# Optimization experiments

Hardware: AMD Instinct MI355X
Metric: run time of the kernel (lower is better)

Reference implementation:

```python
import jax, jax.numpy as jnp
from jax import lax
import numpy as np

B, C, H, W = 8, 256, 128, 128
MID, RMID = C // 2, C // 4          # heatmap-head mid, radius-head mid channels
K = 5                                # K_max centers
THR = 0.1                            # nms_threshold
SMIN, SMAX = 0.05, 0.45              # sigma clamp
BETA = 1.5                           # prior aspect ratio sigma_y/sigma_x
DMAX = 0.08                          # sigma residual max
RMIN, RMAX = 0.03, 0.40              # radius range
BNEPS = 1e-5
PI = float(np.pi)


def setup_inputs() -> dict:
    key = jax.random.key(0)
    ks = jax.random.split(key, 12)
    def n(k, shp, s):
        return jax.random.normal(k, shp, dtype=jnp.float32) * s
    return {
        'x': n(ks[0], (B, C, H, W), 1.0),
        # heatmap head: DWConv3x3 -> PW1x1 -> BN/ReLU -> Conv3x3 -> BN/ReLU -> Conv1x1(+bias=-2) -> Sigmoid
        'hm_dw': n(ks[1], (C, 1, 3, 3), 0.1),
        'hm_pw1': n(ks[2], (MID, C, 1, 1), 0.05),
        'hm_g1': jnp.ones((MID,), jnp.float32), 'hm_b1': jnp.zeros((MID,), jnp.float32),
        'hm_c3': n(ks[3], (MID, MID, 3, 3), 0.05),
        'hm_g2': jnp.ones((MID,), jnp.float32), 'hm_b2': jnp.zeros((MID,), jnp.float32),
        'hm_out_w': n(ks[4], (1, MID, 1, 1), 0.2), 'hm_out_b': jnp.full((1,), -2.0, jnp.float32),
        # radius head: DWConv3x3 -> PW1x1 -> BN/ReLU -> Conv1x1(+bias) -> Sigmoid -> [r_min, r_max]
        'r_dw': n(ks[5], (C, 1, 3, 3), 0.1),
        'r_pw1': n(ks[6], (RMID, C, 1, 1), 0.05),
        'r_g': jnp.ones((RMID,), jnp.float32), 'r_b': jnp.zeros((RMID,), jnp.float32),
        'r_out_w': n(ks[7], (1, RMID, 1, 1), 0.1), 'r_out_b': jnp.zeros((1,), jnp.float32),
        # per-center param predictor
        'log_alpha': jnp.zeros((1,), jnp.float32),
        'mlp_w1': n(ks[8], (C, C // 2), 0.05), 'mlp_b1': jnp.zeros((C // 2,), jnp.float32),
        'mlp_w2': n(ks[9], (C // 2, 4), 0.05), 'mlp_b2': jnp.zeros((4,), jnp.float32),
    }


def conv(x, w, groups=1, pad=0):
    return lax.conv_general_dilated(x, w, (1, 1), [(pad, pad), (pad, pad)],
                                    dimension_numbers=('NCHW', 'OIHW', 'NCHW'),
                                    feature_group_count=groups)


def bn(x, g, b):
    # eval-mode BatchNorm with running_mean=0, running_var=1
    s = g / np.sqrt(1.0 + BNEPS)
    return x * s[:, None, None] + b[:, None, None]


def bilinear_sample(fm, cx, cy):
    # fm: (C,H,W); cx,cy: (K,) normalized in [-1,1]; align_corners=True, border padding
    px = jnp.clip((cx + 1.0) * 0.5 * (W - 1), 0.0, W - 1)
    py = jnp.clip((cy + 1.0) * 0.5 * (H - 1), 0.0, H - 1)
    x0 = jnp.floor(px).astype(jnp.int32); x1 = jnp.minimum(x0 + 1, W - 1)
    y0 = jnp.floor(py).astype(jnp.int32); y1 = jnp.minimum(y0 + 1, H - 1)
    wx = px - x0; wy = py - y0
    v00 = fm[:, y0, x0]; v01 = fm[:, y0, x1]
    v10 = fm[:, y1, x0]; v11 = fm[:, y1, x1]          # (C,K)
    v = (1 - wy) * ((1 - wx) * v00 + wx * v01) + wy * ((1 - wx) * v10 + wx * v11)
    return v.T                                          # (K,C)


def reference(x, hm_dw, hm_pw1, hm_g1, hm_b1, hm_c3, hm_g2, hm_b2, hm_out_w, hm_out_b,
              r_dw, r_pw1, r_g, r_b, r_out_w, r_out_b,
              log_alpha, mlp_w1, mlp_b1, mlp_w2, mlp_b2):
    relu = jax.nn.relu
    # ---- heatmap head ----
    h = conv(x, hm_dw, groups=C, pad=1)
    h = conv(h, hm_pw1)
    h = relu(bn(h, hm_g1, hm_b1))
    h = conv(h, hm_c3, pad=1)
    h = relu(bn(h, hm_g2, hm_b2))
    heat = jax.nn.sigmoid(conv(h, hm_out_w) + hm_out_b[None, :, None, None])  # (B,1,H,W)
    # ---- MaxPool NMS + topk center extraction ----
    pooled = lax.reduce_window(heat, -jnp.inf, lax.max, (1, 1, 3, 3), (1, 1, 1, 1), 'SAME')
    peaks = (heat * (pooled == heat).astype(heat.dtype)).reshape(B, H * W)
    top_vals, top_idx = lax.top_k(peaks, K)             # (B,K)
    valid = (top_vals >= THR).astype(jnp.float32)
    row = (top_idx // W).astype(jnp.float32)
    col = (top_idx % W).astype(jnp.float32)
    ny = 2.0 * row / (H - 1) - 1.0
    nx = 2.0 * col / (W - 1) - 1.0
    centers = lax.stop_gradient(jnp.stack([nx, ny], -1) * valid[..., None])  # (B,K,2)
    # ---- radius map ----
    r = conv(x, r_dw, groups=C, pad=1)
    r = conv(r, r_pw1)
    r = relu(bn(r, r_g, r_b))
    rmap = RMIN + jax.nn.sigmoid(conv(r, r_out_w) + r_out_b[None, :, None, None]) * (RMAX - RMIN)
    # ---- per-center feature/radius sampling + param MLP ----
    cx, cy = centers[..., 0], centers[..., 1]
    feat = jax.vmap(bilinear_sample)(x, cx, cy)          # (B,K,C)
    r_k = jax.vmap(bilinear_sample)(rmap, cx, cy)[..., 0]  # (B,K)
    alpha = jax.nn.softplus(log_alpha)[0]
    p = relu(feat @ mlp_w1 + mlp_b1) @ mlp_w2 + mlp_b2   # (B,K,4)
    dsx = jnp.tanh(p[..., 0]) * DMAX
    dsy = jnp.tanh(p[..., 1]) * DMAX
    theta = jnp.tanh(p[..., 2]) * PI
    wgt = jax.nn.sigmoid(p[..., 3])
    sx = jnp.clip(alpha * r_k + dsx, SMIN, SMAX)
    sy = jnp.clip(alpha * r_k * BETA + dsy, SMIN, SMAX)
    # ---- rotated Gaussian mixture render ----
    yy = jnp.linspace(-1.0, 1.0, H)
    xx = jnp.linspace(-1.0, 1.0, W)
    gy, gx = jnp.meshgrid(yy, xx, indexing='ij')         # (H,W)
    dx = gx[None, None] - cx[..., None, None]            # (B,K,H,W)
    dy = gy[None, None] - cy[..., None, None]
    ct = jnp.cos(theta)[..., None, None]
    st = jnp.sin(theta)[..., None, None]
    xr = ct * dx + st * dy
    yr = -st * dx + ct * dy
    sx4 = sx[..., None, None]; sy4 = sy[..., None, None]
    G = jnp.exp(-(xr ** 2 / (2.0 * sx4 ** 2 + 1e-6) + yr ** 2 / (2.0 * sy4 ** 2 + 1e-6)))
    m = valid[..., None, None]
    mw = wgt[..., None, None] * m                         # (B,K,1,1)
    wsum = jnp.maximum(mw.sum(axis=1, keepdims=True), 1e-6)
    mix = (G * (mw / wsum) * m).sum(axis=1, keepdims=True)  # (B,1,H,W)
    attn = jax.nn.sigmoid(mix * 4.0 - 2.0)
    return jnp.concatenate([attn, heat], axis=1)          # (B,2,H,W)
```

## Files before the change

### kernel.cpp

```cpp
#include <hip/hip_runtime.h>
#include <hip/hip_bf16.h>
#include <math.h>

typedef __hip_bfloat16 bf16;
using short8 = __attribute__((ext_vector_type(8))) short;
using f32x4  = __attribute__((ext_vector_type(4))) float;

#define NB 8
#define NC 256
#define NH 128
#define NW 128
#define NHW 16384
#define MID 128

__device__ __forceinline__ float b2f(bf16 v){ return __bfloat162float(v); }
__device__ __forceinline__ bf16 f2b(float v){ return __float2bfloat16(v); }
#define BN_S 0.9999950000374997f

__global__ __launch_bounds__(256) void k_cvt(const float* __restrict__ src, bf16* __restrict__ dst, int n){
  int i = blockIdx.x*256 + threadIdx.x;
  if(i < n) dst[i] = f2b(src[i]);
}

__global__ __launch_bounds__(256) void k_trans(const float* __restrict__ src, bf16* __restrict__ dst){
  int i = blockIdx.x*256 + threadIdx.x;
  if(i >= MID*MID*9) return;
  int tau = i % 9; int c = (i/9) % MID; int m = i/(9*MID);
  dst[((size_t)tau*MID + m)*MID + c] = f2b(src[i]);
}

__global__ __launch_bounds__(256) void k_dw(const float* __restrict__ x,
                                            const float* __restrict__ w9,
                                            bf16* __restrict__ out){
  __shared__ float tile[10][132];
  int tid = threadIdx.x;
  int c = blockIdx.y, b = blockIdx.z;
  int y0 = blockIdx.x*8;
  const float* xp = x + ((size_t)(b*NC + c))*NHW;
  for(int g = tid; g < 320; g += 256){
    int row = g >> 5, col4 = g & 31;
    int gy = y0 - 1 + row;
    float4 v = make_float4(0.f,0.f,0.f,0.f);
    if(gy >= 0 && gy < NH) v = *(const float4*)(xp + gy*NW + col4*4);
    *(float4*)&tile[row][col4*4] = v;
  }
  float wf[9];
  #pragma unroll
  for(int i=0;i<9;i++) wf[i] = w9[c*9+i];
  __syncthreads();
  int r  = tid >> 5;
  int c0 = (tid & 31)*4;
  float tap[3][6];
  #pragma unroll
  for(int dr=0;dr<3;dr++){
    #pragma unroll
    for(int cc=0;cc<6;cc++){
      int col = c0 - 1 + cc;
      float tv = tile[r+dr][(col<0)?0:((col>127)?127:col)];
      tap[dr][cc] = (col>=0 && col<NW) ? tv : 0.f;
    }
  }
  ushort4 ov;
  ushort* ovp = (ushort*)&ov;
  #pragma unroll
  for(int i=0;i<4;i++){
    float a = 0.f;
    #pragma unroll
    for(int dr=0;dr<3;dr++){
      #pragma unroll
      for(int dc=0;dc<3;dc++) a += tap[dr][i+dc]*wf[dr*3+dc];
    }
    bf16 ab = f2b(a);
    ovp[i] = *(ushort*)&ab;
  }
  *(ushort4*)(out + ((size_t)(b*NC+c))*NHW + (y0+r)*NW + c0) = ov;
}

template<int MT, int MODE>
__global__ __launch_bounds__(256) void k_pw(const bf16* __restrict__ in,
                                            const bf16* __restrict__ wA,
                                            const float* __restrict__ g,
                                            const float* __restrict__ bias,
                                            const float* __restrict__ hw,
                                            const float* __restrict__ hb,
                                            bf16*  __restrict__ outCh,
                                            float* __restrict__ outMap){
  __shared__ ushort ldsB[64][264];
  const int M = MT*16;
  int tid = threadIdx.x;
  int bidx = blockIdx.x;
  int b = bidx >> 8;
  int p0 = (bidx & 255)*64;
  int lane = tid & 63, wave = tid >> 6;
  const ushort* inU = (const ushort*)(in + (size_t)b*NC*NHW);
  const ushort* wU  = (const ushort*)wA;

  #pragma unroll
  for(int gg=0;gg<8;gg++){
    int ch0 = wave*64 + gg*8;
    union { ushort u[8]; short8 v; } t;
    #pragma unroll
    for(int j=0;j<8;j++) t.u[j] = inU[(size_t)(ch0+j)*NHW + p0 + lane];
    *(short8*)&ldsB[lane][ch0] = t.v;
  }
  __syncthreads();

  f32x4 acc[MT];
  #pragma unroll
  for(int i=0;i<MT;i++){
    #pragma unroll
    for(int r=0;r<4;r++) acc[i][r] = 0.f;
  }
  int n = lane & 15, quad = lane >> 4;
  #pragma unroll
  for(int k0=0;k0<NC;k0+=32){
    short8 bfrag = *(const short8*)&ldsB[wave*16 + n][k0 + quad*8];
    #pragma unroll
    for(int mt=0;mt<MT;mt++){
      short8 afrag = *(const short8*)&wU[(size_t)(mt*16 + n)*NC + k0 + quad*8];
      acc[mt] = __builtin_amdgcn_mfma_f32_16x16x32_bf16(afrag, bfrag, acc[mt], 0, 0, 0);
    }
  }

  int pix = p0 + wave*16 + n;
  if(MODE == 0){
    #pragma unroll
    for(int mt=0;mt<MT;mt++){
      #pragma unroll
      for(int r=0;r<4;r++){
        int m = mt*16 + quad*4 + r;
        float v = acc[mt][r]*(g[m]*BN_S) + bias[m];
        outCh[((size_t)(b*M + m))*NHW + pix] = f2b(fmaxf(v, 0.f));
      }
    }
  }else{
    float ph = 0.f;
    #pragma unroll
    for(int mt=0;mt<MT;mt++){
      #pragma unroll
      for(int r=0;r<4;r++){
        int m = mt*16 + quad*4 + r;
        float v = acc[mt][r]*(g[m]*BN_S) + bias[m];
        ph += fmaxf(v, 0.f) * hw[m];
      }
    }
    ph += __shfl_xor(ph, 16);
    ph += __shfl_xor(ph, 32);
    if(lane < 16){
      float sg = 1.f/(1.f + expf(-(ph + hb[0])));
      outMap[(size_t)b*NHW + pix] = 0.03f + sg*0.37f;
    }
  }
}

__global__ __launch_bounds__(256) void k_c3(const bf16* __restrict__ in,
                                            const bf16* __restrict__ wT,
                                            const float* __restrict__ g,
                                            const float* __restrict__ bias,
                                            const float* __restrict__ hw,
                                            const float* __restrict__ hb,
                                            float* __restrict__ heatF,
                                            float* __restrict__ out){
  __shared__ ushort ldsH[66][136];
  int tid = threadIdx.x;
  int bidx = blockIdx.x;
  int b = bidx >> 8;
  int p0 = (bidx & 255)*64;
  int y  = p0 >> 7;
  int x0 = p0 & 127;
  const ushort* inU = (const ushort*)(in + (size_t)b*MID*NHW);
  const ushort* wU  = (const ushort*)wT;
  int lane = tid & 63, wave = tid >> 6;
  int n = lane & 15, quad = lane >> 4;
  f32x4 acc[8];
  #pragma unroll
  for(int i=0;i<8;i++){
    #pragma unroll
    for(int r=0;r<4;r++) acc[i][r] = 0.f;
  }
  for(int dy=0;dy<3;dy++){
    int yy = y + dy - 1;
    bool rowok = (yy>=0) && (yy<NH);
    __syncthreads();
    for(int gg = tid; gg < 1056; gg += 256){
      int col = gg % 66, chg = gg / 66;
      int gcol = x0 - 1 + col;
      bool ok = rowok && (gcol>=0) && (gcol<NW);
      union { ushort u[8]; short8 v; } t;
      #pragma unroll
      for(int j=0;j<8;j++){
        t.u[j] = ok ? inU[(size_t)(chg*8+j)*NHW + yy*NW + gcol] : (ushort)0;
      }
      *(short8*)&ldsH[col][chg*8] = t.v;
    }
    __syncthreads();
    for(int dx=0;dx<3;dx++){
      int tau = dy*3 + dx;
      const ushort* wtb = wU + (size_t)tau*MID*MID;
      #pragma unroll
      for(int k0=0;k0<MID;k0+=32){
        short8 bfrag = *(const short8*)&ldsH[wave*16 + n + dx][k0 + quad*8];
        #pragma unroll
        for(int mt=0;mt<8;mt++){
          short8 afrag = *(const short8*)&wtb[(size_t)(mt*16 + n)*MID + k0 + quad*8];
          acc[mt] = __builtin_amdgcn_mfma_f32_16x16x32_bf16(afrag, bfrag, acc[mt], 0, 0, 0);
        }
      }
    }
  }
  float ph = 0.f;
  #pragma unroll
  for(int mt=0;mt<8;mt++){
    #pragma unroll
    for(int r=0;r<4;r++){
      int m = mt*16 + quad*4 + r;
      float v = acc[mt][r]*(g[m]*BN_S) + bias[m];
      ph += fmaxf(v, 0.f) * hw[m];
    }
  }
  ph += __shfl_xor(ph, 16);
  ph += __shfl_xor(ph, 32);
  if(lane < 16){
    int pix = p0 + wave*16 + lane;
    float sg = 1.f/(1.f + expf(-(ph + hb[0])));
    heatF[(size_t)b*NHW + pix] = sg;
    out[((size_t)(b*2+1))*NHW + pix] = sg;
  }
}

__global__ __launch_bounds__(256) void k_topk1(const float* __restrict__ heat,
                                               float* __restrict__ sv_g,
                                               int*   __restrict__ si_g){
  __shared__ float sv[256*5];
  __shared__ int   si[256*5];
  int blk = blockIdx.x, b = blockIdx.y, tid = threadIdx.x;
  const float* hb = heat + (size_t)b*NHW;
  float tv[5]; int ti[5];
  #pragma unroll
  for(int i=0;i<5;i++){ tv[i] = -1.f; ti[i] = 0x7fffffff; }
  for(int s=0;s<2;s++){
    int p = blk*512 + s*256 + tid;
    int y = p >> 7, x = p & 127;
    float v = hb[p];
    float mx = v;
    for(int dy=-1;dy<=1;dy++){
      int yy = y+dy; if(yy<0||yy>=NH) continue;
      for(int dx=-1;dx<=1;dx++){
        int xc = x+dx; if(xc<0||xc>=NW) continue;
        mx = fmaxf(mx, hb[yy*NW+xc]);
      }
    }
    float pv = (v == mx) ? v : 0.f;
    #pragma unroll
    for(int j=0;j<5;j++){
      if(pv > tv[j] || (pv == tv[j] && p < ti[j])){
        for(int q=4;q>j;q--){ tv[q]=tv[q-1]; ti[q]=ti[q-1]; }
        tv[j] = pv; ti[j] = p;
        break;
      }
    }
  }
  #pragma unroll
  for(int i=0;i<5;i++){ sv[tid*5+i] = tv[i]; si[tid*5+i] = ti[i]; }
  __syncthreads();
  if(tid < 64){
    float mv[5]; int mi[5];
    #pragma unroll
    for(int i=0;i<5;i++){ mv[i] = -1.f; mi[i] = 0x7fffffff; }
    for(int s=0;s<4;s++){
      int t2 = tid + s*64;
      for(int i=0;i<5;i++){
        float pv = sv[t2*5+i]; int pi = si[t2*5+i];
        for(int j=0;j<5;j++){
          if(pv > mv[j] || (pv == mv[j] && pi < mi[j])){
            for(int q=4;q>j;q--){ mv[q]=mv[q-1]; mi[q]=mi[q-1]; }
            mv[j] = pv; mi[j] = pi;
            break;
          }
        }
      }
    }
    for(int i=0;i<5;i++){ sv[tid*5+i] = mv[i]; si[tid*5+i] = mi[i]; }
  }
  __syncthreads();
  if(tid == 0){
    float fv[5]; int fi[5];
    #pragma unroll
    for(int i=0;i<5;i++){ fv[i] = -1.f; fi[i] = 0x7fffffff; }
    for(int t2=0;t2<64;t2++){
      for(int i=0;i<5;i++){
        float pv = sv[t2*5+i]; int pi = si[t2*5+i];
        for(int j=0;j<5;j++){
          if(pv > fv[j] || (pv == fv[j] && pi < fi[j])){
            for(int q=4;q>j;q--){ fv[q]=fv[q-1]; fi[q]=fi[q-1]; }
            fv[j] = pv; fi[j] = pi;
            break;
          }
        }
      }
    }
    for(int i=0;i<5;i++){
      sv_g[(b*32 + blk)*5 + i] = fv[i];
      si_g[(b*32 + blk)*5 + i] = fi[i];
    }
  }
}

__global__ __launch_bounds__(256) void k_topk2(const float* __restrict__ sv_g,
                                               const int*   __restrict__ si_g,
                                               float* __restrict__ centers){
  __shared__ float cv[160];
  __shared__ int   ci[160];
  int b = blockIdx.x, tid = threadIdx.x;
  if(tid < 160){ cv[tid] = sv_g[b*160 + tid]; ci[tid] = si_g[b*160 + tid]; }
  __syncthreads();
  if(tid < 160){
    float v = cv[tid]; int idx = ci[tid];
    int rank = 0;
    for(int j=0;j<160;j++){
      float vj = cv[j]; int ij = ci[j];
      rank += (vj > v || (vj == v && ij < idx)) ? 1 : 0;
    }
    if(rank < 5){
      float valid = (v >= 0.1f) ? 1.f : 0.f;
      float row = (float)(idx >> 7);
      float col = (float)(idx & 127);
      float ny = 2.f*row/127.f - 1.f;
      float nx = 2.f*col/127.f - 1.f;
      float* cp = centers + (b*5+rank)*4;
      cp[0] = nx*valid; cp[1] = ny*valid; cp[2] = v; cp[3] = valid;
    }
  }
}

__global__ __launch_bounds__(256) void k_params(const float* __restrict__ x,
                                                const float* __restrict__ rmap,
                                                const float* __restrict__ centers,
                                                const float* __restrict__ w1,
                                                const float* __restrict__ b1,
                                                const float* __restrict__ w2,
                                                const float* __restrict__ b2,
                                                const float* __restrict__ log_alpha,
                                                float* __restrict__ params){
  __shared__ float feat[NC];
  __shared__ float hmid[128];
  __shared__ float pp[4];
  int b = blockIdx.x, tid = threadIdx.x;
  for(int k=0;k<5;k++){
    float cx = centers[(b*5+k)*4+0];
    float cy = centers[(b*5+k)*4+1];
    float valid = centers[(b*5+k)*4+3];
    float px = fminf(fmaxf((cx+1.f)*0.5f*(NW-1), 0.f), (float)(NW-1));
    float py = fminf(fmaxf((cy+1.f)*0.5f*(NH-1), 0.f), (float)(NH-1));
    int x0 = (int)floorf(px); int x1 = min(x0+1, NW-1);
    int y0 = (int)floorf(py); int y1 = min(y0+1, NH-1);
    float wx = px - (float)x0, wy = py - (float)y0;
    {
      const float* xb = x + ((size_t)b*NC + tid)*NHW;
      float v00 = xb[y0*NW+x0], v01 = xb[y0*NW+x1];
      float v10 = xb[y1*NW+x0], v11 = xb[y1*NW+x1];
      feat[tid] = (1.f-wy)*((1.f-wx)*v00 + wx*v01) + wy*((1.f-wx)*v10 + wx*v11);
    }
    __syncthreads();
    if(tid < 128){
      float a = b1[tid];
      for(int c=0;c<NC;c++) a += feat[c]*w1[c*128+tid];
      hmid[tid] = fmaxf(a, 0.f);
    }
    __syncthreads();
    if(tid < 4){
      float a = b2[tid];
      for(int j=0;j<128;j++) a += hmid[j]*w2[j*4+tid];
      pp[tid] = a;
    }
    __syncthreads();
    if(tid == 0){
      const float* rb = rmap + (size_t)b*NHW;
      float r00 = rb[y0*NW+x0], r01 = rb[y0*NW+x1];
      float r10 = rb[y1*NW+x0], r11 = rb[y1*NW+x1];
      float rk = (1.f-wy)*((1.f-wx)*r00 + wx*r01) + wy*((1.f-wx)*r10 + wx*r11);
      float la = log_alpha[0];
      float alpha = logf(1.f + expf(la));
      float dsx = tanhf(pp[0])*0.08f;
      float dsy = tanhf(pp[1])*0.08f;
      float theta = tanhf(pp[2])*3.14159265358979323846f;
      float wgt = 1.f/(1.f + expf(-pp[3]));
      float sx = fminf(fmaxf(alpha*rk + dsx, 0.05f), 0.45f);
      float sy = fminf(fmaxf(alpha*rk*1.5f + dsy, 0.05f), 0.45f);
      float* P = params + (b*5+k)*8;
      P[0] = cx; P[1] = cy;
      P[2] = cosf(theta); P[3] = sinf(theta);
      P[4] = 1.f/(2.f*sx*sx + 1e-6f);
      P[5] = 1.f/(2.f*sy*sy + 1e-6f);
      P[6] = wgt*valid; P[7] = valid;
    }
    __syncthreads();
  }
}

__global__ __launch_bounds__(256) void k_attn(const float* __restrict__ params,
                                              float* __restrict__ out){
  int tid = threadIdx.x;
  int p = blockIdx.x*256 + tid;
  int b = blockIdx.y;
  int y = p >> 7, x = p & 127;
  float gx = -1.f + 2.f*(float)x/127.f;
  float gy = -1.f + 2.f*(float)y/127.f;
  const float* Pb = params + b*40;
  float wsum = 0.f;
  #pragma unroll
  for(int k=0;k<5;k++) wsum += Pb[k*8+6];
  wsum = fmaxf(wsum, 1e-6f);
  float mix = 0.f;
  #pragma unroll
  for(int k=0;k<5;k++){
    const float* P = Pb + k*8;
    float dx = gx - P[0], dy = gy - P[1];
    float xr =  P[2]*dx + P[3]*dy;
    float yr = -P[3]*dx + P[2]*dy;
    float e = __expf(-(xr*xr*P[4] + yr*yr*P[5]));
    mix += e * (P[6]/wsum);
  }
  float attn = 1.f/(1.f + __expf(-(4.f*mix - 2.f)));
  out[((size_t)(b*2))*NHW + p] = attn;
}

extern "C" void kernel_launch(void* const* d_in, const int* in_sizes, int n_in,
                              void* d_out, int out_size, void* d_ws, size_t ws_size,
                              hipStream_t stream){
  const float* x        = (const float*)d_in[0];
  const float* hm_dw    = (const float*)d_in[1];
  const float* hm_pw1   = (const float*)d_in[2];
  const float* hm_g1    = (const float*)d_in[3];
  const float* hm_b1    = (const float*)d_in[4];
  const float* hm_c3    = (const float*)d_in[5];
  const float* hm_g2    = (const float*)d_in[6];
  const float* hm_b2    = (const float*)d_in[7];
  const float* hm_out_w = (const float*)d_in[8];
  const float* hm_out_b = (const float*)d_in[9];
  const float* r_dw     = (const float*)d_in[10];
  const float* r_pw1    = (const float*)d_in[11];
  const float* r_g      = (const float*)d_in[12];
  const float* r_b      = (const float*)d_in[13];
  const float* r_out_w  = (const float*)d_in[14];
  const float* r_out_b  = (const float*)d_in[15];
  const float* log_alpha= (const float*)d_in[16];
  const float* mlp_w1   = (const float*)d_in[17];
  const float* mlp_b1   = (const float*)d_in[18];
  const float* mlp_w2   = (const float*)d_in[19];
  const float* mlp_b2   = (const float*)d_in[20];
  float* out = (float*)d_out;

  char* ws = (char*)d_ws;
  bf16*  dwX     = (bf16*)ws;
  bf16*  h1      = (bf16*)(ws + 67108864);
  float* heatF   = (float*)(ws + 100663296);
  float* rmapF   = (float*)(ws + 101187584);
  bf16*  wT      = (bf16*)(ws + 101711872);
  bf16*  wPW1h   = (bf16*)(ws + 102006784);
  bf16*  wPW1r   = (bf16*)(ws + 102072320);
  float* tsv     = (float*)(ws + 102105088);
  int*   tsi     = (int*)  (ws + 102110208);
  float* centers = (float*)(ws + 102115328);
  float* params  = (float*)(ws + 102115968);

  k_cvt  <<<dim3(128), dim3(256), 0, stream>>>(hm_pw1, wPW1h, 128*256);
  k_cvt  <<<dim3(64),  dim3(256), 0, stream>>>(r_pw1,  wPW1r, 64*256);
  k_trans<<<dim3(576), dim3(256), 0, stream>>>(hm_c3, wT);

  k_dw<<<dim3(16, NC, NB), dim3(256), 0, stream>>>(x, hm_dw, dwX);
  k_pw<8,0><<<dim3(2048), dim3(256), 0, stream>>>(dwX, wPW1h, hm_g1, hm_b1,
                                                  (const float*)nullptr, (const float*)nullptr,
                                                  h1, (float*)nullptr);
  k_dw<<<dim3(16, NC, NB), dim3(256), 0, stream>>>(x, r_dw, dwX);
  k_pw<4,1><<<dim3(2048), dim3(256), 0, stream>>>(dwX, wPW1r, r_g, r_b,
                                                  r_out_w, r_out_b,
                                                  (bf16*)nullptr, rmapF);
  k_c3<<<dim3(2048), dim3(256), 0, stream>>>(h1, wT, hm_g2, hm_b2, hm_out_w, hm_out_b, heatF, out);
  k_topk1<<<dim3(32, NB), dim3(256), 0, stream>>>(heatF, tsv, tsi);
  k_topk2<<<dim3(NB), dim3(256), 0, stream>>>(tsv, tsi, centers);
  k_params<<<dim3(NB), dim3(256), 0, stream>>>(x, rmapF, centers, mlp_w1, mlp_b1, mlp_w2, mlp_b2, log_alpha, params);
  k_attn<<<dim3(64, NB), dim3(256), 0, stream>>>(params, out);
}
```

Before: 780.4 us.

## Use channel-blocked-by-8 layout for intermediates and load MFMA fragments directly

The depthwise conv now handles 8 channels per block and writes outputs interleaved in groups of 8 channels per pixel, so each 16-byte vector holds the 8 channels of one pixel. The pointwise and 3x3 conv kernels then read their MFMA B fragments straight from global memory as short8 loads, with no LDS staging, transposing gather or barriers. The 3x3 conv now processes a full 128-pixel row per block with two accumulator sets, reusing each weight fragment twice. In exchange it relies on L2/cache for reuse that LDS used to provide, uses more registers for the doubled accumulators, and launches fewer, larger c3 blocks.

```diff
diff --git a/kernel.cpp b/kernel.cpp
--- a/kernel.cpp
+++ b/kernel.cpp
@@ -29,92 +29,84 @@
   dst[((size_t)tau*MID + m)*MID + c] = f2b(src[i]);
 }
 
-__global__ __launch_bounds__(256) void k_dw(const float* __restrict__ x,
-                                            const float* __restrict__ w9,
-                                            bf16* __restrict__ out){
-  __shared__ float tile[10][132];
+__global__ __launch_bounds__(256) void k_dwb(const float* __restrict__ x,
+                                             const float* __restrict__ w9,
+                                             bf16* __restrict__ outB8){
+  __shared__ float tile[8][10][132];
   int tid = threadIdx.x;
-  int c = blockIdx.y, b = blockIdx.z;
+  int cg = blockIdx.y, b = blockIdx.z;
   int y0 = blockIdx.x*8;
-  const float* xp = x + ((size_t)(b*NC + c))*NHW;
-  for(int g = tid; g < 320; g += 256){
-    int row = g >> 5, col4 = g & 31;
+  #pragma unroll
+  for(int it=0; it<10; it++){
+    int idx = it*256 + tid;
+    int c = idx / 320, rem = idx % 320;
+    int row = rem >> 5, col4 = rem & 31;
     int gy = y0 - 1 + row;
     float4 v = make_float4(0.f,0.f,0.f,0.f);
-    if(gy >= 0 && gy < NH) v = *(const float4*)(xp + gy*NW + col4*4);
-    *(float4*)&tile[row][col4*4] = v;
-  }
-  float wf[9];
-  #pragma unroll
-  for(int i=0;i<9;i++) wf[i] = w9[c*9+i];
+    if(gy >= 0 && gy < NH)
+      v = *(const float4*)(x + ((size_t)(b*NC + cg*8 + c))*NHW + gy*NW + col4*4);
+    *(float4*)&tile[c][row][col4*4] = v;
+  }
   __syncthreads();
-  int r  = tid >> 5;
-  int c0 = (tid & 31)*4;
-  float tap[3][6];
-  #pragma unroll
-  for(int dr=0;dr<3;dr++){
-    #pragma unroll
-    for(int cc=0;cc<6;cc++){
-      int col = c0 - 1 + cc;
-      float tv = tile[r+dr][(col<0)?0:((col>127)?127:col)];
-      tap[dr][cc] = (col>=0 && col<NW) ? tv : 0.f;
-    }
-  }
-  ushort4 ov;
-  ushort* ovp = (ushort*)&ov;
+  int row  = tid >> 5;
+  int colb = tid & 31;
+  union { ushort u[8]; short8 v; } o[4];
+  for(int c=0;c<8;c++){
+    float wf[9];
+    #pragma unroll
+    for(int i=0;i<9;i++) wf[i] = w9[(cg*8+c)*9 + i];
+    #pragma unroll
+    for(int i=0;i<4;i++){
+      int col = colb + 32*i;
+      float a = 0.f;
+      #pragma unroll
+      for(int dr=0;dr<3;dr++){
+        #pragma unroll
+        for(int dc=0;dc<3;dc++){
+          int cc = col + dc - 1;
+          float tv = (cc>=0 && cc<NW) ? tile[c][row+dr][cc] : 0.f;
+          a += tv * wf[dr*3+dc];
+        }
+      }
+      bf16 ab = f2b(a);
+      o[i].u[c] = *(ushort*)&ab;
+    }
+  }
   #pragma unroll
   for(int i=0;i<4;i++){
-    float a = 0.f;
-    #pragma unroll
-    for(int dr=0;dr<3;dr++){
-      #pragma unroll
-      for(int dc=0;dc<3;dc++) a += tap[dr][i+dc]*wf[dr*3+dc];
-    }
-    bf16 ab = f2b(a);
-    ovp[i] = *(ushort*)&ab;
-  }
-  *(ushort4*)(out + ((size_t)(b*NC+c))*NHW + (y0+r)*NW + c0) = ov;
+    int col = colb + 32*i;
+    *(short8*)(outB8 + (((size_t)(b*32+cg))*NHW + (y0+row)*NW + col)*8) = o[i].v;
+  }
 }
 
 template<int MT, int MODE>
-__global__ __launch_bounds__(256) void k_pw(const bf16* __restrict__ in,
+__global__ __launch_bounds__(256) void k_pw(const bf16* __restrict__ in8,
                                             const bf16* __restrict__ wA,
                                             const float* __restrict__ g,
                                             const float* __restrict__ bias,
                                             const float* __restrict__ hw,
                                             const float* __restrict__ hb,
-                                            bf16*  __restrict__ outCh,
+                                            bf16*  __restrict__ h1B8,
                                             float* __restrict__ outMap){
-  __shared__ ushort ldsB[64][264];
-  const int M = MT*16;
   int tid = threadIdx.x;
   int bidx = blockIdx.x;
   int b = bidx >> 8;
   int p0 = (bidx & 255)*64;
   int lane = tid & 63, wave = tid >> 6;
-  const ushort* inU = (const ushort*)(in + (size_t)b*NC*NHW);
+  int n = lane & 15, quad = lane >> 4;
+  size_t pix = p0 + wave*16 + n;
+  const ushort* inU = (const ushort*)in8;
   const ushort* wU  = (const ushort*)wA;
 
-  #pragma unroll
-  for(int gg=0;gg<8;gg++){
-    int ch0 = wave*64 + gg*8;
-    union { ushort u[8]; short8 v; } t;
-    #pragma unroll
-    for(int j=0;j<8;j++) t.u[j] = inU[(size_t)(ch0+j)*NHW + p0 + lane];
-    *(short8*)&ldsB[lane][ch0] = t.v;
-  }
-  __syncthreads();
-
   f32x4 acc[MT];
   #pragma unroll
   for(int i=0;i<MT;i++){
     #pragma unroll
     for(int r=0;r<4;r++) acc[i][r] = 0.f;
   }
-  int n = lane & 15, quad = lane >> 4;
   #pragma unroll
   for(int k0=0;k0<NC;k0+=32){
-    short8 bfrag = *(const short8*)&ldsB[wave*16 + n][k0 + quad*8];
+    short8 bfrag = *(const short8*)&inU[ (((size_t)(b*32) + (k0>>3) + quad)*NHW + pix)*8 ];
     #pragma unroll
     for(int mt=0;mt<MT;mt++){
       short8 afrag = *(const short8*)&wU[(size_t)(mt*16 + n)*NC + k0 + quad*8];
@@ -122,16 +114,20 @@
     }
   }
 
-  int pix = p0 + wave*16 + n;
   if(MODE == 0){
     #pragma unroll
     for(int mt=0;mt<MT;mt++){
+      int mg  = mt*2 + (quad>>1);
+      int off = (quad&1)*4;
+      union { ushort u[4]; ushort4 v; } t;
       #pragma unroll
       for(int r=0;r<4;r++){
         int m = mt*16 + quad*4 + r;
         float v = acc[mt][r]*(g[m]*BN_S) + bias[m];
-        outCh[((size_t)(b*M + m))*NHW + pix] = f2b(fmaxf(v, 0.f));
-      }
+        bf16 ab = f2b(fmaxf(v, 0.f));
+        t.u[r] = *(ushort*)&ab;
+      }
+      *(ushort4*)((ushort*)h1B8 + (((size_t)(b*16+mg))*NHW + pix)*8 + off) = t.v;
     }
   }else{
     float ph = 0.f;
@@ -153,7 +149,7 @@
   }
 }
 
-__global__ __launch_bounds__(256) void k_c3(const bf16* __restrict__ in,
+__global__ __launch_bounds__(256) void k_c3(const bf16* __restrict__ h1B8,
                                             const bf16* __restrict__ wT,
                                             const float* __restrict__ g,
                                             const float* __restrict__ bias,
@@ -161,70 +157,67 @@
                                             const float* __restrict__ hb,
                                             float* __restrict__ heatF,
                                             float* __restrict__ out){
-  __shared__ ushort ldsH[66][136];
   int tid = threadIdx.x;
-  int bidx = blockIdx.x;
-  int b = bidx >> 8;
-  int p0 = (bidx & 255)*64;
-  int y  = p0 >> 7;
-  int x0 = p0 & 127;
-  const ushort* inU = (const ushort*)(in + (size_t)b*MID*NHW);
-  const ushort* wU  = (const ushort*)wT;
+  int y = blockIdx.x, b = blockIdx.y;
   int lane = tid & 63, wave = tid >> 6;
   int n = lane & 15, quad = lane >> 4;
-  f32x4 acc[8];
+  const ushort* inU = (const ushort*)h1B8;
+  const ushort* wU  = (const ushort*)wT;
+  f32x4 acc[8][2];
   #pragma unroll
   for(int i=0;i<8;i++){
     #pragma unroll
-    for(int r=0;r<4;r++) acc[i][r] = 0.f;
+    for(int j=0;j<2;j++){
+      #pragma unroll
+      for(int r=0;r<4;r++) acc[i][j][r] = 0.f;
+    }
   }
   for(int dy=0;dy<3;dy++){
     int yy = y + dy - 1;
-    bool rowok = (yy>=0) && (yy<NH);
-    __syncthreads();
-    for(int gg = tid; gg < 1056; gg += 256){
-      int col = gg % 66, chg = gg / 66;
-      int gcol = x0 - 1 + col;
-      bool ok = rowok && (gcol>=0) && (gcol<NW);
-      union { ushort u[8]; short8 v; } t;
-      #pragma unroll
-      for(int j=0;j<8;j++){
-        t.u[j] = ok ? inU[(size_t)(chg*8+j)*NHW + yy*NW + gcol] : (ushort)0;
-      }
-      *(short8*)&ldsH[col][chg*8] = t.v;
-    }
-    __syncthreads();
+    if(yy < 0 || yy >= NH) continue;
     for(int dx=0;dx<3;dx++){
-      int tau = dy*3 + dx;
-      const ushort* wtb = wU + (size_t)tau*MID*MID;
+      const ushort* wtb = wU + (size_t)(dy*3+dx)*MID*MID;
+      int col0 = wave*32 + n + dx - 1;
+      int col1 = col0 + 16;
+      bool ok0 = (col0>=0) && (col0<NW);
+      bool ok1 = (col1>=0) && (col1<NW);
+      size_t rowbase = (size_t)yy*NW;
       #pragma unroll
       for(int k0=0;k0<MID;k0+=32){
-        short8 bfrag = *(const short8*)&ldsH[wave*16 + n + dx][k0 + quad*8];
+        size_t gbase = ((size_t)(b*16) + (k0>>3) + quad)*NHW;
+        short8 b0 = {0,0,0,0,0,0,0,0};
+        short8 b1 = {0,0,0,0,0,0,0,0};
+        if(ok0) b0 = *(const short8*)&inU[(gbase + rowbase + col0)*8];
+        if(ok1) b1 = *(const short8*)&inU[(gbase + rowbase + col1)*8];
         #pragma unroll
         for(int mt=0;mt<8;mt++){
-          short8 afrag = *(const short8*)&wtb[(size_t)(mt*16 + n)*MID + k0 + quad*8];
-          acc[mt] = __builtin_amdgcn_mfma_f32_16x16x32_bf16(afrag, bfrag, acc[mt], 0, 0, 0);
+          short8 a = *(const short8*)&wtb[(size_t)(mt*16 + n)*MID + k0 + quad*8];
+          acc[mt][0] = __builtin_amdgcn_mfma_f32_16x16x32_bf16(a, b0, acc[mt][0], 0, 0, 0);
+          acc[mt][1] = __builtin_amdgcn_mfma_f32_16x16x32_bf16(a, b1, acc[mt][1], 0, 0, 0);
         }
       }
     }
   }
-  float ph = 0.f;
-  #pragma unroll
-  for(int mt=0;mt<8;mt++){
-    #pragma unroll
-    for(int r=0;r<4;r++){
-      int m = mt*16 + quad*4 + r;
-      float v = acc[mt][r]*(g[m]*BN_S) + bias[m];
-      ph += fmaxf(v, 0.f) * hw[m];
-    }
-  }
-  ph += __shfl_xor(ph, 16);
-  ph += __shfl_xor(ph, 32);
-  if(lane < 16){
-    int pix = p0 + wave*16 + lane;
-    float sg = 1.f/(1.f + expf(-(ph + hb[0])));
-    heatF[(size_t)b*NHW + pix] = sg;
-    out[((size_t)(b*2+1))*NHW + pix] = sg;
+  #pragma unroll
+  for(int ng=0;ng<2;ng++){
+    float ph = 0.f;
+    #pragma unroll
+    for(int mt=0;mt<8;mt++){
+      #pragma unroll
+      for(int r=0;r<4;r++){
+        int m = mt*16 + quad*4 + r;
+        float v = acc[mt][ng][r]*(g[m]*BN_S) + bias[m];
+        ph += fmaxf(v, 0.f) * hw[m];
+      }
+    }
+    ph += __shfl_xor(ph, 16);
+    ph += __shfl_xor(ph, 32);
+    if(lane < 16){
+      int pix = y*NW + wave*32 + ng*16 + lane;
+      float sg = 1.f/(1.f + expf(-(ph + hb[0])));
+      heatF[(size_t)b*NHW + pix] = sg;
+      out[((size_t)(b*2+1))*NHW + pix] = sg;
+    }
   }
 }
 
@@ -468,15 +461,15 @@
   k_cvt  <<<dim3(64),  dim3(256), 0, stream>>>(r_pw1,  wPW1r, 64*256);
   k_trans<<<dim3(576), dim3(256), 0, stream>>>(hm_c3, wT);
 
-  k_dw<<<dim3(16, NC, NB), dim3(256), 0, stream>>>(x, hm_dw, dwX);
+  k_dwb<<<dim3(16, 32, NB), dim3(256), 0, stream>>>(x, r_dw, dwX);
+  k_pw<4,1><<<dim3(2048), dim3(256), 0, stream>>>(dwX, wPW1r, r_g, r_b,
+                                                  r_out_w, r_out_b,
+                                                  (bf16*)nullptr, rmapF);
+  k_dwb<<<dim3(16, 32, NB), dim3(256), 0, stream>>>(x, hm_dw, dwX);
   k_pw<8,0><<<dim3(2048), dim3(256), 0, stream>>>(dwX, wPW1h, hm_g1, hm_b1,
                                                   (const float*)nullptr, (const float*)nullptr,
                                                   h1, (float*)nullptr);
-  k_dw<<<dim3(16, NC, NB), dim3(256), 0, stream>>>(x, r_dw, dwX);
-  k_pw<4,1><<<dim3(2048), dim3(256), 0, stream>>>(dwX, wPW1r, r_g, r_b,
-                                                  r_out_w, r_out_b,
-                                                  (bf16*)nullptr, rmapF);
-  k_c3<<<dim3(2048), dim3(256), 0, stream>>>(h1, wT, hm_g2, hm_b2, hm_out_w, hm_out_b, heatF, out);
+  k_c3<<<dim3(128, NB), dim3(256), 0, stream>>>(h1, wT, hm_g2, hm_b2, hm_out_w, hm_out_b, heatF, out);
   k_topk1<<<dim3(32, NB), dim3(256), 0, stream>>>(heatF, tsv, tsi);
   k_topk2<<<dim3(NB), dim3(256), 0, stream>>>(tsv, tsi, centers);
   k_params<<<dim3(NB), dim3(256), 0, stream>>>(x, rmapF, centers, mlp_w1, mlp_b1, mlp_w2, mlp_b2, log_alpha, params);
```

Result: slower. 820.2 us (+5.1%).
